# Kernel optimization log

Hardware: AMD Instinct MI355X
Metric: run time of the kernel (lower is better)

Reference implementation:

```python
import jax, jax.numpy as jnp
import numpy as np


def setup_inputs() -> dict:
    key = jax.random.key(0)
    k1, k2 = jax.random.split(key)
    inputs = jax.random.normal(k1, (16, 64, 64, 64), dtype=jnp.float32)  # NCHW, C=embedding_dim
    codebook = jax.random.normal(k2, (1024, 64), dtype=jnp.float32)      # [K, D]
    return {"inputs": inputs, "codebook": codebook}


def reference(inputs, codebook):
    # inputs: [B, C, H, W] -> [B, H, W, C] -> [N, D]
    D = codebook.shape[1]
    x = jnp.transpose(inputs, (0, 2, 3, 1)).reshape(-1, D)  # [N, D]
    distances = (
        jnp.sum(x * x, axis=1, keepdims=True)
        + jnp.sum(codebook * codebook, axis=1)
        - 2.0 * jnp.matmul(x, codebook.T)
    )
    encoding_indices = jnp.argmin(distances, axis=1)[:, None]  # [N, 1]
    return encoding_indices
```

## Files before the change

kernel.cpp:

```cpp
#include <hip/hip_runtime.h>


typedef float f4 __attribute__((ext_vector_type(4)));
typedef short s8v __attribute__((ext_vector_type(8)));
typedef unsigned int u32;

#define D_DIM 64
#define HW    4096
#define ROWS  64
#define INF_  __builtin_inff()
#define MFMA(a,b,c) __builtin_amdgcn_mfma_f32_16x16x32_bf16(a,b,c,0,0,0)

__device__ __forceinline__ unsigned short bf_rne(float f) {
    u32 u = __builtin_bit_cast(u32, f);
    u32 r = u + 0x7fffu + ((u >> 16) & 1u);
    return (unsigned short)(r >> 16);
}
__device__ __forceinline__ float bf_to_f(unsigned short h) {
    u32 u = ((u32)h) << 16;
    return __builtin_bit_cast(float, u);
}
__device__ __forceinline__ void split3(float f, unsigned short& h,
                                       unsigned short& m, unsigned short& l) {
    h = bf_rne(f);
    float f1 = f - bf_to_f(h);
    m = bf_rne(f1);
    float f2 = f1 - bf_to_f(m);
    l = bf_rne(f2);
}
__device__ __forceinline__ s8v pack8(unsigned short a0, unsigned short a1,
                                     unsigned short a2, unsigned short a3,
                                     unsigned short a4, unsigned short a5,
                                     unsigned short a6, unsigned short a7) {
    uint4 u;
    u.x = a0 | ((u32)a1 << 16);
    u.y = a2 | ((u32)a3 << 16);
    u.z = a4 | ((u32)a5 << 16);
    u.w = a6 | ((u32)a7 << 16);
    return __builtin_bit_cast(s8v, u);
}

__global__ __launch_bounds__(64) void prep_kernel(const float* __restrict__ cb,
                                                  char* __restrict__ wsb) {
    const int blk = blockIdx.x;
    const int lane = threadIdx.x;
    if (blk < 384) {
        const int T = blk / 6;
        const int rem = blk - T * 6;
        const int s = rem / 3;
        const int L = rem - s * 3;
        const int code = T * 16 + (lane & 15);
        const int ch0 = s * 32 + (lane >> 4) * 8;
        const float* src = cb + code * 64 + ch0;
        unsigned short o[8];
#pragma unroll
        for (int j = 0; j < 8; ++j) {
            unsigned short h, m2, l;
            split3(src[j], h, m2, l);
            o[j] = (L == 0) ? h : (L == 1) ? m2 : l;
        }
        uint4 w;
        w.x = o[0] | ((u32)o[1] << 16);
        w.y = o[2] | ((u32)o[3] << 16);
        w.z = o[4] | ((u32)o[5] << 16);
        w.w = o[6] | ((u32)o[7] << 16);
        *(uint4*)(wsb + (size_t)blk * 1024 + lane * 16) = w;
    } else {
        const int k = (blk - 384) * 64 + lane;
        const f4* row = (const f4*)(cb + (size_t)k * 64);
        float sacc = 0.f;
#pragma unroll
        for (int i = 0; i < 16; ++i) {
            f4 v = row[i];
            sacc = fmaf(v.x, v.x, sacc);
            sacc = fmaf(v.y, v.y, sacc);
            sacc = fmaf(v.z, v.z, sacc);
            sacc = fmaf(v.w, v.w, sacc);
        }
        ((float*)(wsb + 384 * 1024))[k] = sacc;
    }
}

#define BUILD_AS(rs, s) {                                                    \
    const float* xr = (const float*)&xs4[(rs) * 16 + m_][0];                 \
    f4 va = *(const f4*)(xr + (s) * 32 + ko);                                \
    f4 vb = *(const f4*)(xr + (s) * 32 + ko + 4);                            \
    unsigned short h0,h1,h2,h3,h4,h5,h6,h7;                                  \
    unsigned short q0,q1,q2,q3,q4,q5,q6,q7;                                  \
    unsigned short l0,l1,l2,l3,l4,l5,l6,l7;                                  \
    split3(-2.f * va.x, h0, q0, l0); split3(-2.f * va.y, h1, q1, l1);        \
    split3(-2.f * va.z, h2, q2, l2); split3(-2.f * va.w, h3, q3, l3);        \
    split3(-2.f * vb.x, h4, q4, l4); split3(-2.f * vb.y, h5, q5, l5);        \
    split3(-2.f * vb.z, h6, q6, l6); split3(-2.f * vb.w, h7, q7, l7);        \
    Ah##rs##s = pack8(h0,h1,h2,h3,h4,h5,h6,h7);                              \
    Am##rs##s = pack8(q0,q1,q2,q3,q4,q5,q6,q7);                              \
    Al##rs##s = pack8(l0,l1,l2,l3,l4,l5,l6,l7);                              \
}

#define LOADB(S, P)                                                          \
    Bh0##S = *(const s8v*)((P) + 0);    Bm0##S = *(const s8v*)((P) + 1024);  \
    Bl0##S = *(const s8v*)((P) + 2048); Bh1##S = *(const s8v*)((P) + 3072);  \
    Bm1##S = *(const s8v*)((P) + 4096); Bl1##S = *(const s8v*)((P) + 5120);

#define MFMA_S(s, BH, BM, BL)                                                \
    acc0 = MFMA(Ah0##s, BH, acc0); acc1 = MFMA(Ah1##s, BH, acc1);            \
    acc2 = MFMA(Ah2##s, BH, acc2); acc3 = MFMA(Ah3##s, BH, acc3);            \
    acc0 = MFMA(Ah0##s, BM, acc0); acc1 = MFMA(Ah1##s, BM, acc1);            \
    acc2 = MFMA(Ah2##s, BM, acc2); acc3 = MFMA(Ah3##s, BM, acc3);            \
    acc0 = MFMA(Am0##s, BH, acc0); acc1 = MFMA(Am1##s, BH, acc1);            \
    acc2 = MFMA(Am2##s, BH, acc2); acc3 = MFMA(Am3##s, BH, acc3);            \
    acc0 = MFMA(Ah0##s, BL, acc0); acc1 = MFMA(Ah1##s, BL, acc1);            \
    acc2 = MFMA(Ah2##s, BL, acc2); acc3 = MFMA(Ah3##s, BL, acc3);            \
    acc0 = MFMA(Am0##s, BM, acc0); acc1 = MFMA(Am1##s, BM, acc1);            \
    acc2 = MFMA(Am2##s, BM, acc2); acc3 = MFMA(Am3##s, BM, acc3);            \
    acc0 = MFMA(Al0##s, BH, acc0); acc1 = MFMA(Al1##s, BH, acc1);            \
    acc2 = MFMA(Al2##s, BH, acc2); acc3 = MFMA(Al3##s, BH, acc3);

#define UPD(rs, i) {                                                         \
    float v = acc##rs[i] + en;                                               \
    bool p = (v < best_##rs##_##i);                                          \
    best_##rs##_##i = p ? v : best_##rs##_##i;                               \
    idx_##rs##_##i  = p ? kn : idx_##rs##_##i;                               \
}
#define EPILOG(TG) {                                                         \
    const int kn = (TG) * 16 + m_;                                           \
    const float en = sEn[kn];                                                \
    UPD(0,0) UPD(0,1) UPD(0,2) UPD(0,3)                                      \
    UPD(1,0) UPD(1,1) UPD(1,2) UPD(1,3)                                      \
    UPD(2,0) UPD(2,1) UPD(2,2) UPD(2,3)                                      \
    UPD(3,0) UPD(3,1) UPD(3,2) UPD(3,3)                                      \
    acc0 = (f4){0.f,0.f,0.f,0.f}; acc1 = (f4){0.f,0.f,0.f,0.f};              \
    acc2 = (f4){0.f,0.f,0.f,0.f}; acc3 = (f4){0.f,0.f,0.f,0.f};              \
}

#define DO_TILE(CUR, NXT, TG, NP) {                                          \
    LOADB(NXT, NP)                                                           \
    MFMA_S(0, Bh0##CUR, Bm0##CUR, Bl0##CUR)                                  \
    MFMA_S(1, Bh1##CUR, Bm1##CUR, Bl1##CUR)                                  \
    EPILOG(TG)                                                               \
}

#define BFLY1(rs, i, msk) {                                                  \
    float ov = __shfl_xor(best_##rs##_##i, msk);                             \
    int   oi = __shfl_xor(idx_##rs##_##i,  msk);                             \
    bool p = (ov < best_##rs##_##i) ||                                       \
             (ov == best_##rs##_##i && oi < idx_##rs##_##i);                 \
    best_##rs##_##i = p ? ov : best_##rs##_##i;                              \
    idx_##rs##_##i  = p ? oi : idx_##rs##_##i;                               \
}
#define BFLY_ALL(msk)                                                        \
    BFLY1(0,0,msk) BFLY1(0,1,msk) BFLY1(0,2,msk) BFLY1(0,3,msk)              \
    BFLY1(1,0,msk) BFLY1(1,1,msk) BFLY1(1,2,msk) BFLY1(1,3,msk)              \
    BFLY1(2,0,msk) BFLY1(2,1,msk) BFLY1(2,2,msk) BFLY1(2,3,msk)              \
    BFLY1(3,0,msk) BFLY1(3,1,msk) BFLY1(3,2,msk) BFLY1(3,3,msk)

#define STORE1(rs, i)                                                        \
    sdq[quarter][(rs) * 16 + rbase + (i)] = best_##rs##_##i;                 \
    siq[quarter][(rs) * 16 + rbase + (i)] = idx_##rs##_##i;

__global__ __launch_bounds__(256, 2) void vq_kernel(const float* __restrict__ x,
                                                    const char* __restrict__ wsb,
                                                    int* __restrict__ out) {
    __shared__ f4    xs4[ROWS][17];
    __shared__ float sEn[1024];
    __shared__ float sdq[4][64];
    __shared__ int   siq[4][64];

    const int tid = threadIdx.x;
    const int lane = tid & 63;
    const int quarter = __builtin_amdgcn_readfirstlane(tid >> 6);
    const int m_ = lane & 15;
    const int ko = (lane >> 4) * 8;
    const int n0 = blockIdx.x * ROWS;
    const int b = n0 >> 12;
    const int hw0 = n0 & (HW - 1);

    const float* enp = (const float*)(wsb + 384 * 1024);
#pragma unroll
    for (int q = 0; q < 4; ++q) sEn[q * 256 + tid] = enp[q * 256 + tid];

    {
        const float* g = x + ((size_t)b * D_DIM + quarter * 16) * HW + hw0 + lane;
        float v[16];
#pragma unroll
        for (int i = 0; i < 16; ++i) v[i] = g[(size_t)i * HW];
#pragma unroll
        for (int j = 0; j < 4; ++j)
            xs4[lane][quarter * 4 + j] = (f4){v[4*j], v[4*j+1], v[4*j+2], v[4*j+3]};
    }
    __syncthreads();

    s8v Ah00, Am00, Al00, Ah01, Am01, Al01;
    s8v Ah10, Am10, Al10, Ah11, Am11, Al11;
    s8v Ah20, Am20, Al20, Ah21, Am21, Al21;
    s8v Ah30, Am30, Al30, Ah31, Am31, Al31;
    BUILD_AS(0,0) BUILD_AS(0,1) BUILD_AS(1,0) BUILD_AS(1,1)
    BUILD_AS(2,0) BUILD_AS(2,1) BUILD_AS(3,0) BUILD_AS(3,1)

    f4 acc0 = (f4){0.f,0.f,0.f,0.f}, acc1 = (f4){0.f,0.f,0.f,0.f};
    f4 acc2 = (f4){0.f,0.f,0.f,0.f}, acc3 = (f4){0.f,0.f,0.f,0.f};
    float best_0_0=INF_, best_0_1=INF_, best_0_2=INF_, best_0_3=INF_;
    float best_1_0=INF_, best_1_1=INF_, best_1_2=INF_, best_1_3=INF_;
    float best_2_0=INF_, best_2_1=INF_, best_2_2=INF_, best_2_3=INF_;
    float best_3_0=INF_, best_3_1=INF_, best_3_2=INF_, best_3_3=INF_;
    int idx_0_0=0, idx_0_1=0, idx_0_2=0, idx_0_3=0;
    int idx_1_0=0, idx_1_1=0, idx_1_2=0, idx_1_3=0;
    int idx_2_0=0, idx_2_1=0, idx_2_2=0, idx_2_3=0;
    int idx_3_0=0, idx_3_1=0, idx_3_2=0, idx_3_3=0;

    s8v Bh0c, Bm0c, Bl0c, Bh1c, Bm1c, Bl1c;
    s8v Bh0n, Bm0n, Bl0n, Bh1n, Bm1n, Bl1n;

    const char* const bp0 = wsb + (size_t)quarter * 98304 + (size_t)lane * 16;
    const char* bp = bp0;
    LOADB(c, bp)
    bp += 6144;

#pragma unroll 1
    for (int tt = 0; tt < 8; ++tt) {
        const int t0 = 2 * tt;
        DO_TILE(c, n, quarter * 16 + t0, bp)
        bp += 6144;
        const char* np = (tt == 7) ? bp0 : bp;
        DO_TILE(n, c, quarter * 16 + t0 + 1, np)
        bp += 6144;
    }

    BFLY_ALL(1) BFLY_ALL(2) BFLY_ALL(4) BFLY_ALL(8)

    if ((lane & 15) == 0) {
        const int rbase = (lane >> 4) * 4;
        STORE1(0,0) STORE1(0,1) STORE1(0,2) STORE1(0,3)
        STORE1(1,0) STORE1(1,1) STORE1(1,2) STORE1(1,3)
        STORE1(2,0) STORE1(2,1) STORE1(2,2) STORE1(2,3)
        STORE1(3,0) STORE1(3,1) STORE1(3,2) STORE1(3,3)
    }
    __syncthreads();

    if (tid < 64) {
        float bv = sdq[0][tid];
        int   bi = siq[0][tid];
#pragma unroll
        for (int q = 1; q < 4; ++q) {
            const float o = sdq[q][tid];
            const int  oi = siq[q][tid];
            if (o < bv) { bv = o; bi = oi; }
        }
        out[n0 + tid] = bi;
    }
}

extern "C" void kernel_launch(void* const* d_in, const int* in_sizes, int n_in,
                              void* d_out, int out_size, void* d_ws, size_t ws_size,
                              hipStream_t stream) {
    const float* x  = (const float*)d_in[0];
    const float* cb = (const float*)d_in[1];
    char* wsb = (char*)d_ws;
    int*  out = (int*)d_out;

    prep_kernel<<<dim3(400), dim3(64), 0, stream>>>(cb, wsb);
    vq_kernel<<<dim3(65536 / ROWS), dim3(256), 0, stream>>>(x, wsb, out);
}
```

Baseline: 111.7 us.

## Share codebook tiles across waves via async global-to-LDS double buffering

After: 108.6 us. 1.03x faster.

```diff
diff --git a/kernel.cpp b/kernel.cpp
--- a/kernel.cpp
+++ b/kernel.cpp
@@ -81,96 +81,97 @@
     }
 }
 
-#define BUILD_AS(rs, s) {                                                    \
-    const float* xr = (const float*)&xs4[(rs) * 16 + m_][0];                 \
-    f4 va = *(const f4*)(xr + (s) * 32 + ko);                                \
-    f4 vb = *(const f4*)(xr + (s) * 32 + ko + 4);                            \
-    unsigned short h0,h1,h2,h3,h4,h5,h6,h7;                                  \
-    unsigned short q0,q1,q2,q3,q4,q5,q6,q7;                                  \
-    unsigned short l0,l1,l2,l3,l4,l5,l6,l7;                                  \
-    split3(-2.f * va.x, h0, q0, l0); split3(-2.f * va.y, h1, q1, l1);        \
-    split3(-2.f * va.z, h2, q2, l2); split3(-2.f * va.w, h3, q3, l3);        \
-    split3(-2.f * vb.x, h4, q4, l4); split3(-2.f * vb.y, h5, q5, l5);        \
-    split3(-2.f * vb.z, h6, q6, l6); split3(-2.f * vb.w, h7, q7, l7);        \
-    Ah##rs##s = pack8(h0,h1,h2,h3,h4,h5,h6,h7);                              \
-    Am##rs##s = pack8(q0,q1,q2,q3,q4,q5,q6,q7);                              \
-    Al##rs##s = pack8(l0,l1,l2,l3,l4,l5,l6,l7);                              \
-}
-
-#define LOADB(S, P)                                                          \
-    Bh0##S = *(const s8v*)((P) + 0);    Bm0##S = *(const s8v*)((P) + 1024);  \
-    Bl0##S = *(const s8v*)((P) + 2048); Bh1##S = *(const s8v*)((P) + 3072);  \
-    Bm1##S = *(const s8v*)((P) + 4096); Bl1##S = *(const s8v*)((P) + 5120);
-
-#define MFMA_S(s, BH, BM, BL)                                                \
-    acc0 = MFMA(Ah0##s, BH, acc0); acc1 = MFMA(Ah1##s, BH, acc1);            \
-    acc2 = MFMA(Ah2##s, BH, acc2); acc3 = MFMA(Ah3##s, BH, acc3);            \
-    acc0 = MFMA(Ah0##s, BM, acc0); acc1 = MFMA(Ah1##s, BM, acc1);            \
-    acc2 = MFMA(Ah2##s, BM, acc2); acc3 = MFMA(Ah3##s, BM, acc3);            \
-    acc0 = MFMA(Am0##s, BH, acc0); acc1 = MFMA(Am1##s, BH, acc1);            \
-    acc2 = MFMA(Am2##s, BH, acc2); acc3 = MFMA(Am3##s, BH, acc3);            \
-    acc0 = MFMA(Ah0##s, BL, acc0); acc1 = MFMA(Ah1##s, BL, acc1);            \
-    acc2 = MFMA(Ah2##s, BL, acc2); acc3 = MFMA(Ah3##s, BL, acc3);            \
-    acc0 = MFMA(Am0##s, BM, acc0); acc1 = MFMA(Am1##s, BM, acc1);            \
-    acc2 = MFMA(Am2##s, BM, acc2); acc3 = MFMA(Am3##s, BM, acc3);            \
-    acc0 = MFMA(Al0##s, BH, acc0); acc1 = MFMA(Al1##s, BH, acc1);            \
-    acc2 = MFMA(Al2##s, BH, acc2); acc3 = MFMA(Al3##s, BH, acc3);
-
-#define UPD(rs, i) {                                                         \
-    float v = acc##rs[i] + en;                                               \
-    bool p = (v < best_##rs##_##i);                                          \
-    best_##rs##_##i = p ? v : best_##rs##_##i;                               \
-    idx_##rs##_##i  = p ? kn : idx_##rs##_##i;                               \
-}
-#define EPILOG(TG) {                                                         \
-    const int kn = (TG) * 16 + m_;                                           \
-    const float en = sEn[kn];                                                \
-    UPD(0,0) UPD(0,1) UPD(0,2) UPD(0,3)                                      \
-    UPD(1,0) UPD(1,1) UPD(1,2) UPD(1,3)                                      \
-    UPD(2,0) UPD(2,1) UPD(2,2) UPD(2,3)                                      \
-    UPD(3,0) UPD(3,1) UPD(3,2) UPD(3,3)                                      \
-    acc0 = (f4){0.f,0.f,0.f,0.f}; acc1 = (f4){0.f,0.f,0.f,0.f};              \
-    acc2 = (f4){0.f,0.f,0.f,0.f}; acc3 = (f4){0.f,0.f,0.f,0.f};              \
-}
-
-#define DO_TILE(CUR, NXT, TG, NP) {                                          \
-    LOADB(NXT, NP)                                                           \
-    MFMA_S(0, Bh0##CUR, Bm0##CUR, Bl0##CUR)                                  \
-    MFMA_S(1, Bh1##CUR, Bm1##CUR, Bl1##CUR)                                  \
-    EPILOG(TG)                                                               \
-}
-
-#define BFLY1(rs, i, msk) {                                                  \
-    float ov = __shfl_xor(best_##rs##_##i, msk);                             \
-    int   oi = __shfl_xor(idx_##rs##_##i,  msk);                             \
-    bool p = (ov < best_##rs##_##i) ||                                       \
-             (ov == best_##rs##_##i && oi < idx_##rs##_##i);                 \
-    best_##rs##_##i = p ? ov : best_##rs##_##i;                              \
-    idx_##rs##_##i  = p ? oi : idx_##rs##_##i;                               \
-}
-#define BFLY_ALL(msk)                                                        \
-    BFLY1(0,0,msk) BFLY1(0,1,msk) BFLY1(0,2,msk) BFLY1(0,3,msk)              \
-    BFLY1(1,0,msk) BFLY1(1,1,msk) BFLY1(1,2,msk) BFLY1(1,3,msk)              \
-    BFLY1(2,0,msk) BFLY1(2,1,msk) BFLY1(2,2,msk) BFLY1(2,3,msk)              \
-    BFLY1(3,0,msk) BFLY1(3,1,msk) BFLY1(3,2,msk) BFLY1(3,3,msk)
-
-#define STORE1(rs, i)                                                        \
-    sdq[quarter][(rs) * 16 + rbase + (i)] = best_##rs##_##i;                 \
-    siq[quarter][(rs) * 16 + rbase + (i)] = idx_##rs##_##i;
-
-__global__ __launch_bounds__(256, 2) void vq_kernel(const float* __restrict__ x,
+__device__ __forceinline__ void gl_lds16(const char* g, char* l) {
+    __builtin_amdgcn_global_load_lds(
+        (const __attribute__((address_space(1))) void*)g,
+        (__attribute__((address_space(3))) void*)l, 16, 0, 0);
+}
+
+#define BUILD_A(s) { \
+    const float* xr = (const float*)&xs4[w16 + m_][0]; \
+    f4 va = *(const f4*)(xr + (s) * 32 + ko); \
+    f4 vb = *(const f4*)(xr + (s) * 32 + ko + 4); \
+    unsigned short h0,h1,h2,h3,h4,h5,h6,h7; \
+    unsigned short q0,q1,q2,q3,q4,q5,q6,q7; \
+    unsigned short l0,l1,l2,l3,l4,l5,l6,l7; \
+    split3(-2.f * va.x, h0, q0, l0); split3(-2.f * va.y, h1, q1, l1); \
+    split3(-2.f * va.z, h2, q2, l2); split3(-2.f * va.w, h3, q3, l3); \
+    split3(-2.f * vb.x, h4, q4, l4); split3(-2.f * vb.y, h5, q5, l5); \
+    split3(-2.f * vb.z, h6, q6, l6); split3(-2.f * vb.w, h7, q7, l7); \
+    Ah##s = pack8(h0,h1,h2,h3,h4,h5,h6,h7); \
+    Am##s = pack8(q0,q1,q2,q3,q4,q5,q6,q7); \
+    Al##s = pack8(l0,l1,l2,l3,l4,l5,l6,l7); \
+}
+
+#define UPD1(t, i, en, kn) { \
+    float v = a##t##a[i] + a##t##b[i] + (en); \
+    bool pr = (v < best##i); \
+    best##i = pr ? v : best##i; \
+    idx##i  = pr ? (kn) : idx##i; \
+}
+
+#define Z4 (f4){0.f,0.f,0.f,0.f}
+
+#define PHASE(CUR, P) { \
+    const char* gsrc = wsb + (size_t)(((P) + 1) & 31) * 12288 + stageoff; \
+    char* ldst = sB + (((CUR) ^ 1) * 12288) + w3072; \
+    gl_lds16(gsrc,        ldst); \
+    gl_lds16(gsrc + 1024, ldst + 1024); \
+    gl_lds16(gsrc + 2048, ldst + 2048); \
+    const char* bb = sB + (CUR) * 12288 + lane16; \
+    s8v B0h0 = *(const s8v*)(bb +     0), B0m0 = *(const s8v*)(bb +  1024); \
+    s8v B0l0 = *(const s8v*)(bb +  2048), B0h1 = *(const s8v*)(bb +  3072); \
+    s8v B0m1 = *(const s8v*)(bb +  4096), B0l1 = *(const s8v*)(bb +  5120); \
+    s8v B1h0 = *(const s8v*)(bb +  6144), B1m0 = *(const s8v*)(bb +  7168); \
+    s8v B1l0 = *(const s8v*)(bb +  8192), B1h1 = *(const s8v*)(bb +  9216); \
+    s8v B1m1 = *(const s8v*)(bb + 10240), B1l1 = *(const s8v*)(bb + 11264); \
+    const float en0 = sEn[(P) * 32 + m_]; \
+    const float en1 = sEn[(P) * 32 + 16 + m_]; \
+    f4 a0a = Z4, a0b = Z4, a1a = Z4, a1b = Z4; \
+    a0a = MFMA(Ah0,B0h0,a0a); a0b = MFMA(Ah1,B0h1,a0b); \
+    a1a = MFMA(Ah0,B1h0,a1a); a1b = MFMA(Ah1,B1h1,a1b); \
+    a0a = MFMA(Ah0,B0m0,a0a); a0b = MFMA(Ah1,B0m1,a0b); \
+    a1a = MFMA(Ah0,B1m0,a1a); a1b = MFMA(Ah1,B1m1,a1b); \
+    a0a = MFMA(Am0,B0h0,a0a); a0b = MFMA(Am1,B0h1,a0b); \
+    a1a = MFMA(Am0,B1h0,a1a); a1b = MFMA(Am1,B1h1,a1b); \
+    a0a = MFMA(Ah0,B0l0,a0a); a0b = MFMA(Ah1,B0l1,a0b); \
+    a1a = MFMA(Ah0,B1l0,a1a); a1b = MFMA(Ah1,B1l1,a1b); \
+    a0a = MFMA(Am0,B0m0,a0a); a0b = MFMA(Am1,B0m1,a0b); \
+    a1a = MFMA(Am0,B1m0,a1a); a1b = MFMA(Am1,B1m1,a1b); \
+    a0a = MFMA(Al0,B0h0,a0a); a0b = MFMA(Al1,B0h1,a0b); \
+    a1a = MFMA(Al0,B1h0,a1a); a1b = MFMA(Al1,B1h1,a1b); \
+    const int kn0 = (P) * 32 + m_; \
+    UPD1(0,0,en0,kn0)    UPD1(0,1,en0,kn0)    UPD1(0,2,en0,kn0)    UPD1(0,3,en0,kn0) \
+    UPD1(1,0,en1,kn0+16) UPD1(1,1,en1,kn0+16) UPD1(1,2,en1,kn0+16) UPD1(1,3,en1,kn0+16) \
+    __syncthreads(); \
+}
+
+#define BF1(i, msk) { \
+    float ov = __shfl_xor(best##i, msk); \
+    int   oi = __shfl_xor(idx##i,  msk); \
+    bool pr = (ov < best##i) || (ov == best##i && oi < idx##i); \
+    best##i = pr ? ov : best##i; \
+    idx##i  = pr ? oi : idx##i; \
+}
+#define BFALL(msk) BF1(0,msk) BF1(1,msk) BF1(2,msk) BF1(3,msk)
+
+__global__ __launch_bounds__(256, 4) void vq_kernel(const float* __restrict__ x,
                                                     const char* __restrict__ wsb,
                                                     int* __restrict__ out) {
-    __shared__ f4    xs4[ROWS][17];
+    __shared__ __align__(16) char smem[24576];
     __shared__ float sEn[1024];
-    __shared__ float sdq[4][64];
-    __shared__ int   siq[4][64];
+    f4 (*xs4)[17] = (f4 (*)[17])smem;
+    char* const sB = smem;
 
     const int tid = threadIdx.x;
     const int lane = tid & 63;
-    const int quarter = __builtin_amdgcn_readfirstlane(tid >> 6);
+    const int w = __builtin_amdgcn_readfirstlane(tid >> 6);
     const int m_ = lane & 15;
     const int ko = (lane >> 4) * 8;
+    const int w16 = w * 16;
+    const int w3072 = w * 3072;
+    const int lane16 = lane * 16;
+    const int stageoff = w3072 + lane16;
     const int n0 = blockIdx.x * ROWS;
     const int b = n0 >> 12;
     const int hw0 = n0 & (HW - 1);
@@ -180,73 +181,43 @@
     for (int q = 0; q < 4; ++q) sEn[q * 256 + tid] = enp[q * 256 + tid];
 
     {
-        const float* g = x + ((size_t)b * D_DIM + quarter * 16) * HW + hw0 + lane;
+        const float* g = x + ((size_t)b * D_DIM + w16) * HW + hw0 + lane;
         float v[16];
 #pragma unroll
         for (int i = 0; i < 16; ++i) v[i] = g[(size_t)i * HW];
 #pragma unroll
         for (int j = 0; j < 4; ++j)
-            xs4[lane][quarter * 4 + j] = (f4){v[4*j], v[4*j+1], v[4*j+2], v[4*j+3]};
+            xs4[lane][w * 4 + j] = (f4){v[4*j], v[4*j+1], v[4*j+2], v[4*j+3]};
     }
     __syncthreads();
 
-    s8v Ah00, Am00, Al00, Ah01, Am01, Al01;
-    s8v Ah10, Am10, Al10, Ah11, Am11, Al11;
-    s8v Ah20, Am20, Al20, Ah21, Am21, Al21;
-    s8v Ah30, Am30, Al30, Ah31, Am31, Al31;
-    BUILD_AS(0,0) BUILD_AS(0,1) BUILD_AS(1,0) BUILD_AS(1,1)
-    BUILD_AS(2,0) BUILD_AS(2,1) BUILD_AS(3,0) BUILD_AS(3,1)
-
-    f4 acc0 = (f4){0.f,0.f,0.f,0.f}, acc1 = (f4){0.f,0.f,0.f,0.f};
-    f4 acc2 = (f4){0.f,0.f,0.f,0.f}, acc3 = (f4){0.f,0.f,0.f,0.f};
-    float best_0_0=INF_, best_0_1=INF_, best_0_2=INF_, best_0_3=INF_;
-    float best_1_0=INF_, best_1_1=INF_, best_1_2=INF_, best_1_3=INF_;
-    float best_2_0=INF_, best_2_1=INF_, best_2_2=INF_, best_2_3=INF_;
-    float best_3_0=INF_, best_3_1=INF_, best_3_2=INF_, best_3_3=INF_;
-    int idx_0_0=0, idx_0_1=0, idx_0_2=0, idx_0_3=0;
-    int idx_1_0=0, idx_1_1=0, idx_1_2=0, idx_1_3=0;
-    int idx_2_0=0, idx_2_1=0, idx_2_2=0, idx_2_3=0;
-    int idx_3_0=0, idx_3_1=0, idx_3_2=0, idx_3_3=0;
-
-    s8v Bh0c, Bm0c, Bl0c, Bh1c, Bm1c, Bl1c;
-    s8v Bh0n, Bm0n, Bl0n, Bh1n, Bm1n, Bl1n;
-
-    const char* const bp0 = wsb + (size_t)quarter * 98304 + (size_t)lane * 16;
-    const char* bp = bp0;
-    LOADB(c, bp)
-    bp += 6144;
+    s8v Ah0, Am0, Al0, Ah1, Am1, Al1;
+    BUILD_A(0) BUILD_A(1)
+    __syncthreads();
+
+    {
+        const char* g0 = wsb + stageoff;
+        char* l0 = sB + w3072;
+        gl_lds16(g0,        l0);
+        gl_lds16(g0 + 1024, l0 + 1024);
+        gl_lds16(g0 + 2048, l0 + 2048);
+    }
+
+    float best0 = INF_, best1 = INF_, best2 = INF_, best3 = INF_;
+    int idx0 = 0, idx1 = 0, idx2 = 0, idx3 = 0;
+    __syncthreads();
 
 #pragma unroll 1
-    for (int tt = 0; tt < 8; ++tt) {
-        const int t0 = 2 * tt;
-        DO_TILE(c, n, quarter * 16 + t0, bp)
-        bp += 6144;
-        const char* np = (tt == 7) ? bp0 : bp;
-        DO_TILE(n, c, quarter * 16 + t0 + 1, np)
-        bp += 6144;
-    }
-
-    BFLY_ALL(1) BFLY_ALL(2) BFLY_ALL(4) BFLY_ALL(8)
-
-    if ((lane & 15) == 0) {
-        const int rbase = (lane >> 4) * 4;
-        STORE1(0,0) STORE1(0,1) STORE1(0,2) STORE1(0,3)
-        STORE1(1,0) STORE1(1,1) STORE1(1,2) STORE1(1,3)
-        STORE1(2,0) STORE1(2,1) STORE1(2,2) STORE1(2,3)
-        STORE1(3,0) STORE1(3,1) STORE1(3,2) STORE1(3,3)
-    }
-    __syncthreads();
-
-    if (tid < 64) {
-        float bv = sdq[0][tid];
-        int   bi = siq[0][tid];
-#pragma unroll
-        for (int q = 1; q < 4; ++q) {
-            const float o = sdq[q][tid];
-            const int  oi = siq[q][tid];
-            if (o < bv) { bv = o; bi = oi; }
-        }
-        out[n0 + tid] = bi;
+    for (int pp = 0; pp < 16; ++pp) {
+        PHASE(0, pp * 2)
+        PHASE(1, pp * 2 + 1)
+    }
+
+    BFALL(1) BFALL(2) BFALL(4) BFALL(8)
+
+    if (m_ == 0) {
+        int4 o4; o4.x = idx0; o4.y = idx1; o4.z = idx2; o4.w = idx3;
+        *(int4*)(out + n0 + w16 + (lane >> 4) * 4) = o4;
     }
 }
 
```
